# Kernel optimization log

Measured on AMD Instinct MI355X. Metric: run time of the kernel, lower is better.

Reference implementation:

```python
import jax, jax.numpy as jnp
import numpy as np

B, T, D, U, V = 256, 200, 512, 1024, 50000


def setup_inputs() -> dict:
    key = jax.random.key(0)
    ks = jax.random.split(key, 8)
    s = lambda k, shape, scale: (jax.random.normal(k, shape, jnp.float32) * scale)
    return {
        "tokens": jax.random.randint(ks[0], (B, T), 0, V, dtype=jnp.int32),
        "emb_table": s(ks[1], (V, D), 0.05),
        "W1": s(ks[2], (D, 4 * U), 0.02),
        "U1": s(ks[3], (U, 4 * U), 0.02),
        "b1": jnp.zeros((4 * U,), jnp.float32),
        "W2": s(ks[4], (U, 4 * U), 0.02),
        "U2": s(ks[5], (U, 4 * U), 0.02),
        "b2": jnp.zeros((4 * U,), jnp.float32),
        "Wfc": s(ks[6], (U, 1), 0.02),
        "bfc": jnp.zeros((1,), jnp.float32),
    }


def _lstm(x, W, Ur, b):
    """x: [B,T,Din] -> (h_seq [B,T,U], h_last [B,U]). Keras gate order i,f,c,o."""
    u = Ur.shape[0]
    xz = jnp.einsum("btd,dg->btg", x, W) + b  # precompute input projections

    def step(carry, zt):
        h, c = carry
        z = zt + h @ Ur  # [B,4U]
        i, f, g, o = jnp.split(z, 4, axis=-1)
        i, f, o = jax.nn.sigmoid(i), jax.nn.sigmoid(f), jax.nn.sigmoid(o)
        c = f * c + i * jnp.tanh(g)
        h = o * jnp.tanh(c)
        return (h, c), h

    h0 = jnp.zeros((x.shape[0], u), x.dtype)
    (h_last, _), h_seq = jax.lax.scan(step, (h0, h0), jnp.swapaxes(xz, 0, 1))
    return jnp.swapaxes(h_seq, 0, 1), h_last


def reference(tokens, emb_table, W1, U1, b1, W2, U2, b2, Wfc, bfc):
    x = emb_table[tokens]                 # [B,T,D]
    h_seq, _ = _lstm(x, W1, U1, b1)       # return_sequences=True
    _, h_last = _lstm(h_seq, W2, U2, b2)  # return last hidden [B,U]
    logits = h_last @ Wfc + bfc           # [B,1]
    return jax.nn.sigmoid(logits)
```

## Files before the change

### kernel.cpp

```cpp
#include <hip/hip_runtime.h>
#include <math.h>

constexpr int kB = 256;
constexpr int kT = 200;
constexpr int kD = 512;
constexpr int kU = 1024;
constexpr int kG = 4096;

typedef short frag8 __attribute__((ext_vector_type(8)));
typedef float floatx4 __attribute__((ext_vector_type(4)));
typedef unsigned short ushort_t;

__device__ __forceinline__ ushort_t f2bf(float f) {
    union { float f; unsigned int u; } v; v.f = f;
    unsigned int r = v.u + 0x7fffu + ((v.u >> 16) & 1u);
    return (ushort_t)(r >> 16);
}
__device__ __forceinline__ float bf2f(ushort_t h) {
    union { unsigned int u; float f; } v; v.u = ((unsigned int)h) << 16;
    return v.f;
}

__global__ __launch_bounds__(256)
void repack_weights(const float* __restrict__ W, const float* __restrict__ Uw,
                    int K1, int K, ushort_t* __restrict__ out)
{
    const int nkb = K >> 5;
    const int kb = blockIdx.x % nkb;
    const int nb = blockIdx.x / nkb;
    __shared__ ushort_t tile[2048];
    const int tid = threadIdx.x;
#pragma unroll
    for (int i = 0; i < 8; i++) {
        int idx  = tid + (i << 8);
        int kl   = idx >> 6;
        int lcol = idx & 63;
        int g  = lcol >> 4;
        int jl = lcol & 15;
        int k  = (kb << 5) + kl;
        int n_old = (g << 10) + (nb << 4) + jl;
        float v = (k < K1) ? W[(long)k * kG + n_old]
                           : Uw[(long)(k - K1) * kG + n_old];
        int n_new_l = (jl << 2) + g;
        int ng = n_new_l >> 4, nl = n_new_l & 15;
        int quad = kl >> 3, e = kl & 7;
        tile[ng * 512 + (quad * 16 + nl) * 8 + e] = f2bf(v);
    }
    __syncthreads();
    long base = ((long)(nb * nkb + kb)) * 2048;
    *(frag8*)&out[base + tid * 8] = *(frag8*)&tile[tid * 8];
}

__global__ __launch_bounds__(256)
void repack_bias(const float* __restrict__ b1, const float* __restrict__ b2,
                 float* __restrict__ o1, float* __restrict__ o2)
{
    int n = blockIdx.x * blockDim.x + threadIdx.x;
    int n_old = ((n & 3) << 10) + (n >> 2);
    o1[n] = b1[n_old];
    o2[n] = b2[n_old];
}

__global__ __launch_bounds__(128)
void xgather(const int* __restrict__ tokens, const float* __restrict__ emb,
             ushort_t* __restrict__ xbf)
{
    int bt = blockIdx.x;
    int tok = tokens[bt];
    float4 v = *(const float4*)(emb + (long)tok * kD + threadIdx.x * 4);
    unsigned int lo = ((unsigned int)f2bf(v.y) << 16) | f2bf(v.x);
    unsigned int hi = ((unsigned int)f2bf(v.w) << 16) | f2bf(v.z);
    uint2 p; p.x = lo; p.y = hi;
    *(uint2*)(xbf + (long)bt * kD + threadIdx.x * 4) = p;
}

struct Batch { frag8 A[8]; frag8 B[16]; };

template<int K1BK>
__device__ __forceinline__ void load_batch(int b, Batch& bb,
    const ushort_t* a1p0, const ushort_t* a1p1,
    const ushort_t* a2p0, const ushort_t* a2p1,
    const frag8* wbase)
{
    const int kb0 = b * 4;
    if (kb0 < K1BK) {
#pragma unroll
        for (int u = 0; u < 4; u++) {
            const frag8* wp = wbase + (kb0 + u) * 256;
            bb.B[u*4+0] = wp[0];   bb.B[u*4+1] = wp[64];
            bb.B[u*4+2] = wp[128]; bb.B[u*4+3] = wp[192];
            bb.A[u*2+0] = *(const frag8*)(a1p0 + (kb0 + u) * 32);
            bb.A[u*2+1] = *(const frag8*)(a1p1 + (kb0 + u) * 32);
        }
    } else {
#pragma unroll
        for (int u = 0; u < 4; u++) {
            const frag8* wp = wbase + (kb0 + u) * 256;
            bb.B[u*4+0] = wp[0];   bb.B[u*4+1] = wp[64];
            bb.B[u*4+2] = wp[128]; bb.B[u*4+3] = wp[192];
            bb.A[u*2+0] = *(const frag8*)(a2p0 + (kb0 - K1BK + u) * 32);
            bb.A[u*2+1] = *(const frag8*)(a2p1 + (kb0 - K1BK + u) * 32);
        }
    }
}

__device__ __forceinline__ void mfma_batch(const Batch& bb, floatx4 acc[2][4])
{
#pragma unroll
    for (int u = 0; u < 4; u++)
#pragma unroll
        for (int mi = 0; mi < 2; mi++)
#pragma unroll
            for (int ct = 0; ct < 4; ct++)
                acc[mi][ct] = __builtin_amdgcn_mfma_f32_16x16x32_bf16(
                    bb.A[u*2+mi], bb.B[u*4+ct], acc[mi][ct], 0, 0, 0);
}

template<int NKB, int K1BK>
__device__ __forceinline__ void step_core(
    const ushort_t* __restrict__ A1, long a1_rs, long a1_off,
    const ushort_t* __restrict__ A2,
    const ushort_t* __restrict__ Wp,
    const float4* __restrict__ biasP4,
    float* __restrict__ cSt, ushort_t* __restrict__ hOut,
    float* __restrict__ zsw)
{
    const int tid  = threadIdx.x;
    const int lane = tid & 63;
    const int wave = tid >> 6;
    const int nb2  = blockIdx.x * 2 + (wave & 1);
    const int wrow = (blockIdx.y << 6) + ((wave >> 1) << 5);
    const int kq   = (lane >> 4) << 3;

    const int r0 = wrow + (lane & 15);
    const ushort_t* a1p0 = A1 + (long)r0 * a1_rs + a1_off + kq;
    const ushort_t* a1p1 = A1 + (long)(r0 + 16) * a1_rs + a1_off + kq;
    const ushort_t* a2p0 = A2 + (long)r0 * kU + kq;
    const ushort_t* a2p1 = A2 + (long)(r0 + 16) * kU + kq;
    const frag8* wbase = (const frag8*)Wp + (long)nb2 * (NKB * 256) + lane;

    floatx4 acc[2][4];
#pragma unroll
    for (int i = 0; i < 2; i++)
#pragma unroll
        for (int j = 0; j < 4; j++) acc[i][j] = (floatx4){0.f, 0.f, 0.f, 0.f};

    constexpr int NBATCH = NKB / 4;
    Batch X, Y;
    load_batch<K1BK>(0, X, a1p0, a1p1, a2p0, a2p1, wbase);
#pragma unroll 1
    for (int b = 0; b < NBATCH; b += 2) {
        load_batch<K1BK>(b + 1, Y, a1p0, a1p1, a2p0, a2p1, wbase);
        mfma_batch(X, acc);
        if (b + 2 < NBATCH)
            load_batch<K1BK>(b + 2, X, a1p0, a1p1, a2p0, a2p1, wbase);
        mfma_batch(Y, acc);
    }

    const int q = lane >> 4, c16 = lane & 15;
#pragma unroll 1
    for (int mi = 0; mi < 2; mi++) {
#pragma unroll
        for (int ct = 0; ct < 4; ct++)
#pragma unroll
            for (int r = 0; r < 4; r++)
                zsw[((q << 2) + r) * 68 + (ct << 4) + c16] = acc[mi][ct][r];
#pragma unroll
        for (int ii = 0; ii < 4; ii++) {
            int cell = lane + (ii << 6);
            int rowl = cell >> 4, jl = cell & 15;
            float4 z4 = *(float4*)&zsw[rowl * 68 + (jl << 2)];
            float4 bv = biasP4[(nb2 << 4) + jl];
            float zi = z4.x + bv.x, zf = z4.y + bv.y;
            float zg = z4.z + bv.z, zo = z4.w + bv.w;
            float ig = 1.f / (1.f + __expf(-zi));
            float fg = 1.f / (1.f + __expf(-zf));
            float og = 1.f / (1.f + __expf(-zo));
            float gg = 1.f - 2.f / (__expf(2.f * zg) + 1.f);
            int m = wrow + (mi << 4) + rowl;
            long ci = (long)m * kU + (nb2 << 4) + jl;
            float cn = fg * cSt[ci] + ig * gg;
            float tc = 1.f - 2.f / (__expf(2.f * cn) + 1.f);
            cSt[ci] = cn;
            hOut[ci] = f2bf(og * tc);
        }
    }
}

__global__ __launch_bounds__(256, 1)
void lstm_merged(int zmask,
    const ushort_t* h1_for2, const ushort_t* h2prev, const ushort_t* W2p,
    const float* b2p, float* c2, ushort_t* h2out,
    const ushort_t* xbf, int t1,
    const ushort_t* h1prev, const ushort_t* W1p,
    const float* b1p, float* c1, ushort_t* h1out)
{
    __shared__ __align__(16) float zs[4][16 * 68];
    float* zsw = zs[threadIdx.x >> 6];
    if (blockIdx.z == 0) {
        if (!(zmask & 1)) return;
        step_core<64, 32>(h1_for2, kU, 0, h2prev, W2p,
                          (const float4*)b2p, c2, h2out, zsw);
    } else {
        if (!(zmask & 2)) return;
        step_core<48, 16>(xbf, (long)kT * kD, (long)t1 * kD, h1prev, W1p,
                          (const float4*)b1p, c1, h1out, zsw);
    }
}

__global__ __launch_bounds__(256)
void fc_sigmoid(const ushort_t* __restrict__ h, const float* __restrict__ Wfc,
                const float* __restrict__ bfc, float* __restrict__ out)
{
    int b = blockIdx.x, tid = threadIdx.x;
    float s = 0.f;
    for (int j = tid; j < kU; j += 256) s += bf2f(h[(long)b * kU + j]) * Wfc[j];
    __shared__ float red[4];
    for (int off = 32; off > 0; off >>= 1) s += __shfl_down(s, off, 64);
    if ((tid & 63) == 0) red[tid >> 6] = s;
    __syncthreads();
    if (tid == 0) {
        float t = red[0] + red[1] + red[2] + red[3] + bfc[0];
        out[b] = 1.f / (1.f + expf(-t));
    }
}

extern "C" void kernel_launch(void* const* d_in, const int* in_sizes, int n_in,
                              void* d_out, int out_size, void* d_ws, size_t ws_size,
                              hipStream_t stream)
{
    (void)in_sizes; (void)n_in; (void)out_size; (void)ws_size;

    const int*   tokens = (const int*)d_in[0];
    const float* emb    = (const float*)d_in[1];
    const float* W1     = (const float*)d_in[2];
    const float* U1     = (const float*)d_in[3];
    const float* b1     = (const float*)d_in[4];
    const float* W2     = (const float*)d_in[5];
    const float* U2     = (const float*)d_in[6];
    const float* b2     = (const float*)d_in[7];
    const float* Wfc    = (const float*)d_in[8];
    const float* bfc    = (const float*)d_in[9];
    float* out = (float*)d_out;

    ushort_t* W1p = (ushort_t*)d_ws;
    ushort_t* W2p = W1p + (size_t)1536 * kG;
    float* b1p = (float*)(W2p + (size_t)2048 * kG);
    float* b2p = b1p + kG;
    float* c1  = b2p + kG;
    float* c2  = c1 + (size_t)kB * kU;
    ushort_t* hbuf = (ushort_t*)(c2 + (size_t)kB * kU);
    ushort_t* h1b[2] = { hbuf, hbuf + (size_t)kB * kU };
    ushort_t* h2b[2] = { hbuf + 2 * (size_t)kB * kU, hbuf + 3 * (size_t)kB * kU };
    ushort_t* xbf = hbuf + 4 * (size_t)kB * kU;

    repack_weights<<<48 * 64, 256, 0, stream>>>(W1, U1, 512, 1536, W1p);
    repack_weights<<<64 * 64, 256, 0, stream>>>(W2, U2, 1024, 2048, W2p);
    repack_bias<<<16, 256, 0, stream>>>(b1, b2, b1p, b2p);
    xgather<<<kB * kT, 128, 0, stream>>>(tokens, emb, xbf);
    hipMemsetAsync(c1, 0, (size_t)kB * kU * (2 * 4 + 4 * 2), stream);

    for (int l = 0; l <= kT; l++) {
        int t2 = l - 1, t1 = l;
        int zmask = (t2 >= 0 ? 1 : 0) | (t1 < kT ? 2 : 0);
        lstm_merged<<<dim3(32, 4, 2), 256, 0, stream>>>(zmask,
            h1b[(t2 + 1) & 1], h2b[t2 & 1], W2p, b2p, c2, h2b[(t2 + 1) & 1],
            xbf, t1, h1b[t1 & 1], W1p, b1p, c1, h1b[(t1 + 1) & 1]);
    }

    fc_sigmoid<<<kB, 256, 0, stream>>>(h2b[0], Wfc, bfc, out);
}
```

Measured before the change: 5.870 ms.

## Make LSTM a persistent cooperative kernel with LDS-resident weights and grid barriers

Replaces the 201 per-timestep kernel launches with one cooperative persistent kernel of 256 blocks. Each block loads its slice of the recurrent and input weights into shared memory once, holds its cell state in registers, and steps through time using an atomic-counter grid barrier. This removes repeated weight reads from global memory and L2, the per-step cell-state traffic, and launch overhead. In exchange it adds a spin-wait barrier on every step and needs 128KB+ of LDS per block, with one block per CU.

New measurement: 8.770 ms. 1.49x slower.

```diff
diff --git a/kernel.cpp b/kernel.cpp
--- a/kernel.cpp
+++ b/kernel.cpp
@@ -74,137 +74,182 @@
     *(uint2*)(xbf + (long)bt * kD + threadIdx.x * 4) = p;
 }
 
-struct Batch { frag8 A[8]; frag8 B[16]; };
-
-template<int K1BK>
-__device__ __forceinline__ void load_batch(int b, Batch& bb,
-    const ushort_t* a1p0, const ushort_t* a1p1,
-    const ushort_t* a2p0, const ushort_t* a2p1,
-    const frag8* wbase)
-{
-    const int kb0 = b * 4;
-    if (kb0 < K1BK) {
-#pragma unroll
-        for (int u = 0; u < 4; u++) {
-            const frag8* wp = wbase + (kb0 + u) * 256;
-            bb.B[u*4+0] = wp[0];   bb.B[u*4+1] = wp[64];
-            bb.B[u*4+2] = wp[128]; bb.B[u*4+3] = wp[192];
-            bb.A[u*2+0] = *(const frag8*)(a1p0 + (kb0 + u) * 32);
-            bb.A[u*2+1] = *(const frag8*)(a1p1 + (kb0 + u) * 32);
-        }
+struct Batch { frag8 A[16]; frag8 B[8]; };
+
+template<int K1KB>
+__device__ __forceinline__ void load_batch(int bi, Batch& bb,
+    const ushort_t* const (&a1p)[4], const ushort_t* const (&a2p)[4],
+    const frag8* __restrict__ wl)
+{
+    const int kb0 = bi * 4;
+#pragma unroll
+    for (int u = 0; u < 4; u++) {
+        const int kb = kb0 + u;
+        bb.B[u*2+0] = wl[(kb*2+0) * 64];
+        bb.B[u*2+1] = wl[(kb*2+1) * 64];
+    }
+    if (kb0 < K1KB) {
+#pragma unroll
+        for (int u = 0; u < 4; u++)
+#pragma unroll
+            for (int i = 0; i < 4; i++)
+                bb.A[u*4+i] = *(const frag8*)(a1p[i] + (kb0+u) * 32);
     } else {
 #pragma unroll
-        for (int u = 0; u < 4; u++) {
-            const frag8* wp = wbase + (kb0 + u) * 256;
-            bb.B[u*4+0] = wp[0];   bb.B[u*4+1] = wp[64];
-            bb.B[u*4+2] = wp[128]; bb.B[u*4+3] = wp[192];
-            bb.A[u*2+0] = *(const frag8*)(a2p0 + (kb0 - K1BK + u) * 32);
-            bb.A[u*2+1] = *(const frag8*)(a2p1 + (kb0 - K1BK + u) * 32);
-        }
-    }
-}
-
-__device__ __forceinline__ void mfma_batch(const Batch& bb, floatx4 acc[2][4])
+        for (int u = 0; u < 4; u++)
+#pragma unroll
+            for (int i = 0; i < 4; i++)
+                bb.A[u*4+i] = *(const frag8*)(a2p[i] + (kb0+u-K1KB) * 32);
+    }
+}
+
+__device__ __forceinline__ void mfma_batch(const Batch& bb, floatx4 (&acc)[4][2])
 {
 #pragma unroll
     for (int u = 0; u < 4; u++)
 #pragma unroll
-        for (int mi = 0; mi < 2; mi++)
-#pragma unroll
-            for (int ct = 0; ct < 4; ct++)
+        for (int mi = 0; mi < 4; mi++)
+#pragma unroll
+            for (int ct = 0; ct < 2; ct++)
                 acc[mi][ct] = __builtin_amdgcn_mfma_f32_16x16x32_bf16(
-                    bb.A[u*2+mi], bb.B[u*4+ct], acc[mi][ct], 0, 0, 0);
-}
-
-template<int NKB, int K1BK>
-__device__ __forceinline__ void step_core(
+                    bb.A[u*4+mi], bb.B[u*2+ct], acc[mi][ct], 0, 0, 0);
+}
+
+__device__ __forceinline__ void grid_sync(unsigned* __restrict__ bar, unsigned target)
+{
+    __syncthreads();
+    if (threadIdx.x == 0) {
+        __hip_atomic_fetch_add(bar, 1u, __ATOMIC_RELEASE, __HIP_MEMORY_SCOPE_AGENT);
+        while (__hip_atomic_load(bar, __ATOMIC_RELAXED, __HIP_MEMORY_SCOPE_AGENT) < target)
+            __builtin_amdgcn_s_sleep(2);
+        __builtin_amdgcn_fence(__ATOMIC_ACQUIRE, "agent");
+    }
+    __syncthreads();
+}
+
+template<int NKB, int K1KB>
+__device__ __forceinline__ void step_block(
     const ushort_t* __restrict__ A1, long a1_rs, long a1_off,
     const ushort_t* __restrict__ A2,
-    const ushort_t* __restrict__ Wp,
-    const float4* __restrict__ biasP4,
-    float* __restrict__ cSt, ushort_t* __restrict__ hOut,
-    float* __restrict__ zsw)
-{
-    const int tid  = threadIdx.x;
-    const int lane = tid & 63;
-    const int wave = tid >> 6;
-    const int nb2  = blockIdx.x * 2 + (wave & 1);
-    const int wrow = (blockIdx.y << 6) + ((wave >> 1) << 5);
-    const int kq   = (lane >> 4) << 3;
-
+    const ushort_t* __restrict__ wlds_,
+    float4 bias4, float (&creg)[4][2],
+    ushort_t* __restrict__ hOut, int ub, float* __restrict__ zsw)
+{
+    const int tid = threadIdx.x, lane = tid & 63, wave = tid >> 6;
+    const int wrow = wave << 6;
     const int r0 = wrow + (lane & 15);
-    const ushort_t* a1p0 = A1 + (long)r0 * a1_rs + a1_off + kq;
-    const ushort_t* a1p1 = A1 + (long)(r0 + 16) * a1_rs + a1_off + kq;
-    const ushort_t* a2p0 = A2 + (long)r0 * kU + kq;
-    const ushort_t* a2p1 = A2 + (long)(r0 + 16) * kU + kq;
-    const frag8* wbase = (const frag8*)Wp + (long)nb2 * (NKB * 256) + lane;
-
-    floatx4 acc[2][4];
-#pragma unroll
-    for (int i = 0; i < 2; i++)
-#pragma unroll
-        for (int j = 0; j < 4; j++) acc[i][j] = (floatx4){0.f, 0.f, 0.f, 0.f};
+    const int kq = (lane >> 4) << 3;
+
+    const ushort_t* a1p[4]; const ushort_t* a2p[4];
+#pragma unroll
+    for (int i = 0; i < 4; i++) {
+        a1p[i] = A1 + (long)(r0 + 16*i) * a1_rs + a1_off + kq;
+        a2p[i] = A2 + (long)(r0 + 16*i) * kU + kq;
+    }
+    const frag8* wl = (const frag8*)wlds_ + lane;
+
+    floatx4 acc[4][2];
+#pragma unroll
+    for (int i = 0; i < 4; i++) {
+        acc[i][0] = (floatx4){0.f,0.f,0.f,0.f};
+        acc[i][1] = (floatx4){0.f,0.f,0.f,0.f};
+    }
 
     constexpr int NBATCH = NKB / 4;
     Batch X, Y;
-    load_batch<K1BK>(0, X, a1p0, a1p1, a2p0, a2p1, wbase);
+    load_batch<K1KB>(0, X, a1p, a2p, wl);
 #pragma unroll 1
-    for (int b = 0; b < NBATCH; b += 2) {
-        load_batch<K1BK>(b + 1, Y, a1p0, a1p1, a2p0, a2p1, wbase);
+    for (int bi = 0; bi < NBATCH; bi += 2) {
+        load_batch<K1KB>(bi + 1, Y, a1p, a2p, wl);
         mfma_batch(X, acc);
-        if (b + 2 < NBATCH)
-            load_batch<K1BK>(b + 2, X, a1p0, a1p1, a2p0, a2p1, wbase);
+        if (bi + 2 < NBATCH) load_batch<K1KB>(bi + 2, X, a1p, a2p, wl);
         mfma_batch(Y, acc);
     }
 
     const int q = lane >> 4, c16 = lane & 15;
-#pragma unroll 1
-    for (int mi = 0; mi < 2; mi++) {
-#pragma unroll
-        for (int ct = 0; ct < 4; ct++)
+    const int rl0 = lane >> 3, jl = lane & 7;
+#pragma unroll
+    for (int mi = 0; mi < 4; mi++) {
+#pragma unroll
+        for (int ct = 0; ct < 2; ct++)
 #pragma unroll
             for (int r = 0; r < 4; r++)
-                zsw[((q << 2) + r) * 68 + (ct << 4) + c16] = acc[mi][ct][r];
-#pragma unroll
-        for (int ii = 0; ii < 4; ii++) {
-            int cell = lane + (ii << 6);
-            int rowl = cell >> 4, jl = cell & 15;
-            float4 z4 = *(float4*)&zsw[rowl * 68 + (jl << 2)];
-            float4 bv = biasP4[(nb2 << 4) + jl];
-            float zi = z4.x + bv.x, zf = z4.y + bv.y;
-            float zg = z4.z + bv.z, zo = z4.w + bv.w;
+                zsw[((q << 2) + r) * 36 + (ct << 4) + c16] = acc[mi][ct][r];
+#pragma unroll
+        for (int ii = 0; ii < 2; ii++) {
+            int rowl = rl0 + (ii << 3);
+            float4 z4 = *(float4*)&zsw[rowl * 36 + (jl << 2)];
+            float zi = z4.x + bias4.x, zf = z4.y + bias4.y;
+            float zg = z4.z + bias4.z, zo = z4.w + bias4.w;
             float ig = 1.f / (1.f + __expf(-zi));
             float fg = 1.f / (1.f + __expf(-zf));
             float og = 1.f / (1.f + __expf(-zo));
             float gg = 1.f - 2.f / (__expf(2.f * zg) + 1.f);
+            float cn = fg * creg[mi][ii] + ig * gg;
+            creg[mi][ii] = cn;
+            float tc = 1.f - 2.f / (__expf(2.f * cn) + 1.f);
             int m = wrow + (mi << 4) + rowl;
-            long ci = (long)m * kU + (nb2 << 4) + jl;
-            float cn = fg * cSt[ci] + ig * gg;
-            float tc = 1.f - 2.f / (__expf(2.f * cn) + 1.f);
-            cSt[ci] = cn;
-            hOut[ci] = f2bf(og * tc);
+            hOut[(long)m * kU + ub + jl] = f2bf(og * tc);
         }
     }
 }
 
 __global__ __launch_bounds__(256, 1)
-void lstm_merged(int zmask,
-    const ushort_t* h1_for2, const ushort_t* h2prev, const ushort_t* W2p,
-    const float* b2p, float* c2, ushort_t* h2out,
-    const ushort_t* xbf, int t1,
-    const ushort_t* h1prev, const ushort_t* W1p,
-    const float* b1p, float* c1, ushort_t* h1out)
-{
-    __shared__ __align__(16) float zs[4][16 * 68];
-    float* zsw = zs[threadIdx.x >> 6];
-    if (blockIdx.z == 0) {
-        if (!(zmask & 1)) return;
-        step_core<64, 32>(h1_for2, kU, 0, h2prev, W2p,
-                          (const float4*)b2p, c2, h2out, zsw);
-    } else {
-        if (!(zmask & 2)) return;
-        step_core<48, 16>(xbf, (long)kT * kD, (long)t1 * kD, h1prev, W1p,
-                          (const float4*)b1p, c1, h1out, zsw);
+void lstm_persist(const ushort_t* __restrict__ W1p, const ushort_t* __restrict__ W2p,
+                  const float* __restrict__ b1p, const float* __restrict__ b2p,
+                  const ushort_t* __restrict__ xbf,
+                  ushort_t* __restrict__ h1a, ushort_t* __restrict__ h1b,
+                  ushort_t* __restrict__ h2a, ushort_t* __restrict__ h2b,
+                  unsigned* __restrict__ bar)
+{
+    __shared__ __align__(16) ushort_t wlds[65536];
+    __shared__ __align__(16) float zs[4][576];
+
+    const int bid = blockIdx.x;
+    const bool isL2 = bid < 128;
+    const int b = isL2 ? bid : bid - 128;
+    const int tid = threadIdx.x, lane = tid & 63, wave = tid >> 6;
+
+    {
+        const frag8* wg = (const frag8*)(isL2 ? W2p : W1p);
+        const int NKB = isL2 ? 64 : 48;
+        const int nb2 = b >> 1, cbase = (b & 1) * 2;
+        const long gb = (long)nb2 * NKB * 256;
+        frag8* wl = (frag8*)wlds;
+        for (int i = tid; i < NKB * 128; i += 256) {
+            int kb = i >> 7, r = i & 127;
+            wl[i] = wg[gb + ((long)kb * 4 + cbase + (r >> 6)) * 64 + (r & 63)];
+        }
+    }
+
+    const float4* biasP4 = (const float4*)(isL2 ? b2p : b1p);
+    const float4 bias4 = biasP4[b * 8 + (lane & 7)];
+
+    float creg[4][2];
+#pragma unroll
+    for (int i = 0; i < 4; i++) { creg[i][0] = 0.f; creg[i][1] = 0.f; }
+
+    float* zsw = zs[wave];
+    const int ub = b << 3;
+
+    __syncthreads();
+
+#pragma unroll 1
+    for (int l = 0; l <= kT; l++) {
+        ushort_t* h1cur = (l & 1) ? h1b : h1a;
+        ushort_t* h1nxt = (l & 1) ? h1a : h1b;
+        ushort_t* h2prv = (l & 1) ? h2a : h2b;
+        ushort_t* h2cur = (l & 1) ? h2b : h2a;
+        if (isL2) {
+            if (l >= 1)
+                step_block<64, 32>(h1cur, kU, 0, h2prv, wlds,
+                                   bias4, creg, h2cur, ub, zsw);
+        } else {
+            if (l < kT)
+                step_block<48, 16>(xbf, (long)kT * kD, (long)l * kD, h1cur, wlds,
+                                   bias4, creg, h1nxt, ub, zsw);
+        }
+        grid_sync(bar, 256u * (unsigned)(l + 1));
     }
 }
 
@@ -247,26 +292,24 @@
     ushort_t* W2p = W1p + (size_t)1536 * kG;
     float* b1p = (float*)(W2p + (size_t)2048 * kG);
     float* b2p = b1p + kG;
-    float* c1  = b2p + kG;
-    float* c2  = c1 + (size_t)kB * kU;
-    ushort_t* hbuf = (ushort_t*)(c2 + (size_t)kB * kU);
-    ushort_t* h1b[2] = { hbuf, hbuf + (size_t)kB * kU };
-    ushort_t* h2b[2] = { hbuf + 2 * (size_t)kB * kU, hbuf + 3 * (size_t)kB * kU };
-    ushort_t* xbf = hbuf + 4 * (size_t)kB * kU;
+    ushort_t* hbuf = (ushort_t*)(b2p + kG);
+    ushort_t* h1a = hbuf;
+    ushort_t* h1b = hbuf + (size_t)kB * kU;
+    ushort_t* h2a = hbuf + 2 * (size_t)kB * kU;
+    ushort_t* h2b = hbuf + 3 * (size_t)kB * kU;
+    unsigned* bar = (unsigned*)(hbuf + 4 * (size_t)kB * kU);
+    ushort_t* xbf = (ushort_t*)(bar + 16);
 
     repack_weights<<<48 * 64, 256, 0, stream>>>(W1, U1, 512, 1536, W1p);
     repack_weights<<<64 * 64, 256, 0, stream>>>(W2, U2, 1024, 2048, W2p);
     repack_bias<<<16, 256, 0, stream>>>(b1, b2, b1p, b2p);
     xgather<<<kB * kT, 128, 0, stream>>>(tokens, emb, xbf);
-    hipMemsetAsync(c1, 0, (size_t)kB * kU * (2 * 4 + 4 * 2), stream);
-
-    for (int l = 0; l <= kT; l++) {
-        int t2 = l - 1, t1 = l;
-        int zmask = (t2 >= 0 ? 1 : 0) | (t1 < kT ? 2 : 0);
-        lstm_merged<<<dim3(32, 4, 2), 256, 0, stream>>>(zmask,
-            h1b[(t2 + 1) & 1], h2b[t2 & 1], W2p, b2p, c2, h2b[(t2 + 1) & 1],
-            xbf, t1, h1b[t1 & 1], W1p, b1p, c1, h1b[(t1 + 1) & 1]);
-    }
-
-    fc_sigmoid<<<kB, 256, 0, stream>>>(h2b[0], Wfc, bfc, out);
-}
+    hipMemsetAsync(hbuf, 0, 4 * (size_t)kB * kU * sizeof(ushort_t) + 64, stream);
+
+    void* args[] = { &W1p, &W2p, &b1p, &b2p, &xbf,
+                     &h1a, &h1b, &h2a, &h2b, &bar };
+    hipLaunchCooperativeKernel((void*)lstm_persist, dim3(256), dim3(256),
+                               args, 0, stream);
+
+    fc_sigmoid<<<kB, 256, 0, stream>>>(h2a, Wfc, bfc, out);
+}
```

## Stage weight tiles in double-buffered LDS shared across all batch rows

Applied to the files above, without the earlier changes.

Each block now owns one gate-column group and all 256 batch rows, using 8 waves of 512 threads instead of 4 row groups of 256-thread blocks. Weight fragments are loaded cooperatively once into a double-buffered LDS tile and shared by all waves, instead of each wave streaming them from global memory. This cuts the repeated global/L2 weight reads that came from the same columns being fetched by four row blocks. The cost is a block barrier per K-chunk, more LDS use, and fewer, larger blocks per launch.

Result: slower. 8.166 ms (+39.1%).

```diff
diff --git a/kernel.cpp b/kernel.cpp
--- a/kernel.cpp
+++ b/kernel.cpp
@@ -74,70 +74,30 @@
     *(uint2*)(xbf + (long)bt * kD + threadIdx.x * 4) = p;
 }
 
-struct Batch { frag8 A[8]; frag8 B[16]; };
-
-template<int K1BK>
-__device__ __forceinline__ void load_batch(int b, Batch& bb,
-    const ushort_t* a1p0, const ushort_t* a1p1,
-    const ushort_t* a2p0, const ushort_t* a2p1,
-    const frag8* wbase)
-{
-    const int kb0 = b * 4;
-    if (kb0 < K1BK) {
-#pragma unroll
-        for (int u = 0; u < 4; u++) {
-            const frag8* wp = wbase + (kb0 + u) * 256;
-            bb.B[u*4+0] = wp[0];   bb.B[u*4+1] = wp[64];
-            bb.B[u*4+2] = wp[128]; bb.B[u*4+3] = wp[192];
-            bb.A[u*2+0] = *(const frag8*)(a1p0 + (kb0 + u) * 32);
-            bb.A[u*2+1] = *(const frag8*)(a1p1 + (kb0 + u) * 32);
-        }
-    } else {
-#pragma unroll
-        for (int u = 0; u < 4; u++) {
-            const frag8* wp = wbase + (kb0 + u) * 256;
-            bb.B[u*4+0] = wp[0];   bb.B[u*4+1] = wp[64];
-            bb.B[u*4+2] = wp[128]; bb.B[u*4+3] = wp[192];
-            bb.A[u*2+0] = *(const frag8*)(a2p0 + (kb0 - K1BK + u) * 32);
-            bb.A[u*2+1] = *(const frag8*)(a2p1 + (kb0 - K1BK + u) * 32);
-        }
-    }
-}
-
-__device__ __forceinline__ void mfma_batch(const Batch& bb, floatx4 acc[2][4])
-{
-#pragma unroll
-    for (int u = 0; u < 4; u++)
-#pragma unroll
-        for (int mi = 0; mi < 2; mi++)
-#pragma unroll
-            for (int ct = 0; ct < 4; ct++)
-                acc[mi][ct] = __builtin_amdgcn_mfma_f32_16x16x32_bf16(
-                    bb.A[u*2+mi], bb.B[u*4+ct], acc[mi][ct], 0, 0, 0);
-}
-
-template<int NKB, int K1BK>
+template<int NKB, int K1KB>
 __device__ __forceinline__ void step_core(
     const ushort_t* __restrict__ A1, long a1_rs, long a1_off,
     const ushort_t* __restrict__ A2,
     const ushort_t* __restrict__ Wp,
     const float4* __restrict__ biasP4,
     float* __restrict__ cSt, ushort_t* __restrict__ hOut,
-    float* __restrict__ zsw)
+    ushort_t* __restrict__ bl, float* __restrict__ zsw)
 {
     const int tid  = threadIdx.x;
     const int lane = tid & 63;
     const int wave = tid >> 6;
-    const int nb2  = blockIdx.x * 2 + (wave & 1);
-    const int wrow = (blockIdx.y << 6) + ((wave >> 1) << 5);
+    const int nb2  = blockIdx.x;
+    const int wrow = wave << 5;
     const int kq   = (lane >> 4) << 3;
-
-    const int r0 = wrow + (lane & 15);
+    const int r0   = wrow + (lane & 15);
+
     const ushort_t* a1p0 = A1 + (long)r0 * a1_rs + a1_off + kq;
     const ushort_t* a1p1 = A1 + (long)(r0 + 16) * a1_rs + a1_off + kq;
     const ushort_t* a2p0 = A2 + (long)r0 * kU + kq;
     const ushort_t* a2p1 = A2 + (long)(r0 + 16) * kU + kq;
-    const frag8* wbase = (const frag8*)Wp + (long)nb2 * (NKB * 256) + lane;
+
+    const ushort_t* Wg = Wp + (long)nb2 * NKB * 2048;
+    constexpr int NCH = NKB / 4;
 
     floatx4 acc[2][4];
 #pragma unroll
@@ -145,16 +105,70 @@
 #pragma unroll
         for (int j = 0; j < 4; j++) acc[i][j] = (floatx4){0.f, 0.f, 0.f, 0.f};
 
-    constexpr int NBATCH = NKB / 4;
-    Batch X, Y;
-    load_batch<K1BK>(0, X, a1p0, a1p1, a2p0, a2p1, wbase);
+    auto ldA = [&](int ch, frag8 (&d)[8]) {
+        const int kb0 = ch * 4;
+        if (kb0 < K1KB) {
+#pragma unroll
+            for (int u = 0; u < 4; u++) {
+                d[u*2+0] = *(const frag8*)(a1p0 + (kb0 + u) * 32);
+                d[u*2+1] = *(const frag8*)(a1p1 + (kb0 + u) * 32);
+            }
+        } else {
+#pragma unroll
+            for (int u = 0; u < 4; u++) {
+                d[u*2+0] = *(const frag8*)(a2p0 + (kb0 - K1KB + u) * 32);
+                d[u*2+1] = *(const frag8*)(a2p1 + (kb0 - K1KB + u) * 32);
+            }
+        }
+    };
+
+    auto one = [&](int ch, frag8 (&cur)[8], frag8 (&nxt)[8]) {
+        const int p = ch & 1;
+        const bool pf = (ch + 1 < NCH);
+        frag8 g0, g1;
+        if (pf) {
+            const ushort_t* gs = Wg + (long)(ch + 1) * 8192 + tid * 16;
+            g0 = *(const frag8*)gs;
+            g1 = *(const frag8*)(gs + 8);
+            ldA(ch + 1, nxt);
+        }
+        const ushort_t* bp = bl + p * 8192;
+#pragma unroll
+        for (int kbl = 0; kbl < 4; kbl++) {
+            frag8 b0 = *(const frag8*)&bp[((kbl*4+0)*64 + lane) * 8];
+            frag8 b1 = *(const frag8*)&bp[((kbl*4+1)*64 + lane) * 8];
+            frag8 b2 = *(const frag8*)&bp[((kbl*4+2)*64 + lane) * 8];
+            frag8 b3 = *(const frag8*)&bp[((kbl*4+3)*64 + lane) * 8];
+#pragma unroll
+            for (int mi = 0; mi < 2; mi++) {
+                acc[mi][0] = __builtin_amdgcn_mfma_f32_16x16x32_bf16(cur[kbl*2+mi], b0, acc[mi][0], 0, 0, 0);
+                acc[mi][1] = __builtin_amdgcn_mfma_f32_16x16x32_bf16(cur[kbl*2+mi], b1, acc[mi][1], 0, 0, 0);
+                acc[mi][2] = __builtin_amdgcn_mfma_f32_16x16x32_bf16(cur[kbl*2+mi], b2, acc[mi][2], 0, 0, 0);
+                acc[mi][3] = __builtin_amdgcn_mfma_f32_16x16x32_bf16(cur[kbl*2+mi], b3, acc[mi][3], 0, 0, 0);
+            }
+        }
+        if (pf) {
+            *(frag8*)&bl[(p ^ 1) * 8192 + tid * 16]     = g0;
+            *(frag8*)&bl[(p ^ 1) * 8192 + tid * 16 + 8] = g1;
+        }
+        __syncthreads();
+    };
+
+    frag8 aX[8], aY[8];
+    {
+        const ushort_t* gs = Wg + tid * 16;
+        frag8 g0 = *(const frag8*)gs;
+        frag8 g1 = *(const frag8*)(gs + 8);
+        ldA(0, aX);
+        *(frag8*)&bl[tid * 16]     = g0;
+        *(frag8*)&bl[tid * 16 + 8] = g1;
+    }
+    __syncthreads();
+
 #pragma unroll 1
-    for (int b = 0; b < NBATCH; b += 2) {
-        load_batch<K1BK>(b + 1, Y, a1p0, a1p1, a2p0, a2p1, wbase);
-        mfma_batch(X, acc);
-        if (b + 2 < NBATCH)
-            load_batch<K1BK>(b + 2, X, a1p0, a1p1, a2p0, a2p1, wbase);
-        mfma_batch(Y, acc);
+    for (int c = 0; c < NCH; c += 2) {
+        one(c,     aX, aY);
+        one(c + 1, aY, aX);
     }
 
     const int q = lane >> 4, c16 = lane & 15;
@@ -187,7 +201,7 @@
     }
 }
 
-__global__ __launch_bounds__(256, 1)
+__global__ __launch_bounds__(512, 2)
 void lstm_merged(int zmask,
     const ushort_t* h1_for2, const ushort_t* h2prev, const ushort_t* W2p,
     const float* b2p, float* c2, ushort_t* h2out,
@@ -195,16 +209,17 @@
     const ushort_t* h1prev, const ushort_t* W1p,
     const float* b1p, float* c1, ushort_t* h1out)
 {
-    __shared__ __align__(16) float zs[4][16 * 68];
+    __shared__ __align__(16) ushort_t bl[16384];
+    __shared__ __align__(16) float zs[8][1088];
     float* zsw = zs[threadIdx.x >> 6];
     if (blockIdx.z == 0) {
         if (!(zmask & 1)) return;
         step_core<64, 32>(h1_for2, kU, 0, h2prev, W2p,
-                          (const float4*)b2p, c2, h2out, zsw);
+                          (const float4*)b2p, c2, h2out, bl, zsw);
     } else {
         if (!(zmask & 2)) return;
         step_core<48, 16>(xbf, (long)kT * kD, (long)t1 * kD, h1prev, W1p,
-                          (const float4*)b1p, c1, h1out, zsw);
+                          (const float4*)b1p, c1, h1out, bl, zsw);
     }
 }
 
@@ -263,7 +278,7 @@
     for (int l = 0; l <= kT; l++) {
         int t2 = l - 1, t1 = l;
         int zmask = (t2 >= 0 ? 1 : 0) | (t1 < kT ? 2 : 0);
-        lstm_merged<<<dim3(32, 4, 2), 256, 0, stream>>>(zmask,
+        lstm_merged<<<dim3(64, 1, 2), 512, 0, stream>>>(zmask,
             h1b[(t2 + 1) & 1], h2b[t2 & 1], W2p, b2p, c2, h2b[(t2 + 1) & 1],
             xbf, t1, h1b[t1 & 1], W1p, b1p, c1, h1b[(t1 + 1) & 1]);
     }
```
